# Kernel tuning notes

Hardware: AMD Instinct MI355X
Metric: run time of the kernel (lower is better)

## Reference

```python
import jax, jax.numpy as jnp
import numpy as np

N = 10000
E = 640000
IN_CH = 512
OUT_CH = 256
K = 2


def setup_inputs() -> dict:
    key = jax.random.key(0)
    k1, k2, k3, k4, k5 = jax.random.split(key, 5)
    x = jax.random.normal(k1, (N, IN_CH), dtype=jnp.float32)
    edge_index = jax.random.randint(k2, (2, E), 0, N, dtype=jnp.int64)
    lin_w = jax.random.normal(k3, (OUT_CH, IN_CH), dtype=jnp.float32) * (1.0 / np.sqrt(IN_CH))
    lin_b = jax.random.normal(k4, (OUT_CH,), dtype=jnp.float32) * 0.01
    weights = jax.random.uniform(k5, (K,), dtype=jnp.float32)
    return {"x": x, "edge_index": edge_index, "lin_w": lin_w, "lin_b": lin_b, "weights": weights}


def reference(x, edge_index, lin_w, lin_b, weights):
    n = x.shape[0]
    row, col = edge_index[0], edge_index[1]
    # deg = bincount(row); symmetric-normalized edge weights
    deg = jax.ops.segment_sum(jnp.ones(row.shape[0], dtype=x.dtype), row, num_segments=n)
    deg_inv_sqrt = jnp.where(deg > 0, jax.lax.rsqrt(deg), 0.0)
    norm = deg_inv_sqrt[row] * deg_inv_sqrt[col]  # [E]

    def spmm(h):
        # y[i] = sum_{e: row[e]==i} norm[e] * h[col[e]]
        return jax.ops.segment_sum(norm[:, None] * h[col], row, num_segments=n)

    out = x @ lin_w.T + lin_b  # [N, OUT_CH]
    # Faithful ARMA loop: x_k starts from the CURRENT accumulated `out` each hop-group
    for k in range(K):
        x_k = out
        for _ in range(k + 1):
            x_k = spmm(x_k)
        out = out + weights[k] * x_k
    return out
```

## Files before the change

### kernel.cpp

```cpp
#include <hip/hip_runtime.h>

#define N_NODES 10000
#define E_EDGES 640000
#define IN_CH   512
#define OUT_CH  256
#define HALF_CH 128
#define CSR_CAP (E_EDGES + 16 * N_NODES + 128)
#define G_GEMM_X 157
#define G_GEMM  (G_GEMM_X * 2)
#define HBLK    125
#define EPB     5120
#define CNT_LD  128

typedef short bf16x8 __attribute__((ext_vector_type(8)));
typedef float f32x4  __attribute__((ext_vector_type(4)));

__device__ __forceinline__ unsigned short f2b(float f) {
    unsigned int u = __float_as_uint(f);
    return (unsigned short)((u + 0x7FFFu + ((u >> 16) & 1u)) >> 16);
}
__device__ __forceinline__ float lo16(unsigned int u) { return __uint_as_float(u << 16); }
__device__ __forceinline__ float hi16(unsigned int u) { return __uint_as_float(u & 0xFFFF0000u); }
__device__ __forceinline__ float b2f(unsigned short u) { return __uint_as_float(((unsigned int)u) << 16); }

__global__ __launch_bounds__(256) void hist_rank(const int* __restrict__ row,
                                                 int* __restrict__ cnt,
                                                 unsigned short* __restrict__ rank) {
    __shared__ int hist[N_NODES];
    int b = blockIdx.x, tid = threadIdx.x;
    for (int i = tid; i < N_NODES; i += 256) hist[i] = 0;
    __syncthreads();
    int ebase = b * EPB;
    #pragma unroll 4
    for (int i = tid; i < EPB; i += 256) {
        int r = row[ebase + i];
        rank[ebase + i] = (unsigned short)atomicAdd(&hist[r], 1);
    }
    __syncthreads();
    for (int i = tid; i < N_NODES; i += 256) cnt[(size_t)i * CNT_LD + b] = hist[i];
}

__global__ __launch_bounds__(256) void alloc_a(int* __restrict__ cnt,
                                               int2* __restrict__ pd,
                                               float* __restrict__ dinv, float* __restrict__ sq,
                                               int* __restrict__ pads, int n) {
    int r = blockIdx.x * 4 + (threadIdx.x >> 6);
    int lane = threadIdx.x & 63;
    if (r >= n) return;
    int* cr = cnt + (size_t)r * CNT_LD;
    int v0 = cr[lane];
    int v1 = (lane < HBLK - 64) ? cr[64 + lane] : 0;
    int s0 = v0, s1 = v1;
    #pragma unroll
    for (int off = 1; off < 64; off <<= 1) {
        int t0 = __shfl_up(s0, off, 64);
        int t1 = __shfl_up(s1, off, 64);
        if (lane >= off) { s0 += t0; s1 += t1; }
    }
    int tot0 = __shfl(s0, 63, 64);
    int d = tot0 + __shfl(s1, 63, 64);
    int pad = (d + 15) & ~15;
    cr[lane] = s0 - v0;
    if (lane < HBLK - 64) cr[64 + lane] = tot0 + s1 - v1;
    if (lane == 0) {
        dinv[r] = (d > 0) ? rsqrtf((float)d) : 0.0f;
        sq[r]   = (d > 0) ? sqrtf((float)d) : 0.0f;
        pd[r] = make_int2(d, pad);
        pads[r] = pad;
    }
}

__global__ __launch_bounds__(1024) void scan_pads(const int* __restrict__ pads,
                                                  int* __restrict__ rowstart, int n) {
    __shared__ int ls[1024];
    int t = threadIdx.x;
    int base = t * 10;
    int loc[10];
    int sum = 0;
    if (base < n) {
        #pragma unroll
        for (int i = 0; i < 10; i++) { loc[i] = pads[base + i]; sum += loc[i]; }
    }
    ls[t] = sum;
    __syncthreads();
    for (int off = 1; off < 1024; off <<= 1) {
        int v = (t >= off) ? ls[t - off] : 0;
        __syncthreads();
        ls[t] += v;
        __syncthreads();
    }
    if (base < n) {
        int run = ls[t] - sum;
        #pragma unroll
        for (int i = 0; i < 10; i++) { rowstart[base + i] = run; run += loc[i]; }
    }
}

__global__ __launch_bounds__(256) void alloc_b(int* __restrict__ cnt,
                                               const int* __restrict__ rowstart,
                                               const int2* __restrict__ pd,
                                               int2* __restrict__ seg,
                                               int* __restrict__ csr_col, int n) {
    int r = blockIdx.x * 4 + (threadIdx.x >> 6);
    int lane = threadIdx.x & 63;
    if (r >= n) return;
    int s = rowstart[r];
    int2 pd_ = pd[r];
    int* cr = cnt + (size_t)r * CNT_LD;
    cr[lane] += s;
    if (lane < HBLK - 64) cr[64 + lane] += s;
    if (lane == 0) seg[r] = make_int2(s, s + pd_.y);
    int j = pd_.x + lane;
    if (j < pd_.y) csr_col[s + j] = N_NODES;
}

__global__ __launch_bounds__(256) void gemm_scatter(const float* __restrict__ x,
                                                    const float* __restrict__ w,
                                                    const float* __restrict__ bias,
                                                    const float* __restrict__ dinv,
                                                    unsigned short* __restrict__ h0b,
                                                    const int* __restrict__ row,
                                                    const int* __restrict__ col,
                                                    const int* __restrict__ base,
                                                    const unsigned short* __restrict__ rank,
                                                    int* __restrict__ csr_col) {
    __shared__ unsigned short As[64][72];
    __shared__ unsigned short Bs[128][72];
    int bid = blockIdx.x;
    int tid = threadIdx.x;
    if (bid >= G_GEMM) {
        int sb = bid - G_GEMM;
        int ebase = sb * EPB;
        #pragma unroll 4
        for (int i = tid; i < EPB; i += 256) {
            int e = ebase + i;
            int r = row[e];
            int p = base[(size_t)r * CNT_LD + sb] + (int)rank[e];
            csr_col[p] = col[e];
        }
        return;
    }
    int bx = bid % G_GEMM_X;
    int plane = bid / G_GEMM_X;
    int wave = tid >> 6, lane = tid & 63, quad = lane >> 4, l16 = lane & 15;
    int row0 = bx * 64;
    int n0 = plane * 128;
    unsigned short* h0b_p = h0b + (size_t)plane * (N_NODES + 1) * HALF_CH;

    int ar = tid >> 2;
    int aseg = (tid & 3) * 16;
    int br = tid >> 1;
    int bseg = (tid & 1) * 32;

    f32x4 acc[8] = {};
    for (int k0 = 0; k0 < IN_CH; k0 += 64) {
        {
            int gr = row0 + ar;
            if (gr < N_NODES) {
                const float4* src = (const float4*)(x + (size_t)gr * IN_CH + k0 + aseg);
                #pragma unroll
                for (int i = 0; i < 4; i++) {
                    float4 v = src[i];
                    ushort4 o;
                    o.x = f2b(v.x); o.y = f2b(v.y); o.z = f2b(v.z); o.w = f2b(v.w);
                    *(ushort4*)&As[ar][aseg + i * 4] = o;
                }
            } else {
                ushort4 z = {0, 0, 0, 0};
                #pragma unroll
                for (int i = 0; i < 4; i++) *(ushort4*)&As[ar][aseg + i * 4] = z;
            }
        }
        {
            const float4* src = (const float4*)(w + (size_t)(n0 + br) * IN_CH + k0 + bseg);
            #pragma unroll
            for (int i = 0; i < 8; i++) {
                float4 v = src[i];
                ushort4 o;
                o.x = f2b(v.x); o.y = f2b(v.y); o.z = f2b(v.z); o.w = f2b(v.w);
                *(ushort4*)&Bs[br][bseg + i * 4] = o;
            }
        }
        __syncthreads();
        #pragma unroll
        for (int kk = 0; kk < 2; kk++) {
            bf16x8 a = *(const bf16x8*)&As[wave * 16 + l16][kk * 32 + quad * 8];
            #pragma unroll
            for (int t = 0; t < 8; t++) {
                bf16x8 b = *(const bf16x8*)&Bs[t * 16 + l16][kk * 32 + quad * 8];
                acc[t] = __builtin_amdgcn_mfma_f32_16x16x32_bf16(a, b, acc[t], 0, 0, 0);
            }
        }
        __syncthreads();
    }
    #pragma unroll
    for (int t = 0; t < 8; t++) {
        int lcol = t * 16 + l16;
        int col_ = n0 + lcol;
        float bv = bias[col_];
        #pragma unroll
        for (int r = 0; r < 4; r++) {
            int grow = row0 + wave * 16 + quad * 4 + r;
            if (grow < N_NODES) {
                float v = acc[t][r] + bv;
                h0b_p[(size_t)grow * HALF_CH + lcol] = f2b(v * dinv[grow]);
            }
        }
    }
    if (bx == 0 && tid < 64)
        ((unsigned int*)(h0b_p + (size_t)N_NODES * HALF_CH))[tid] = 0u;
}

__global__ __launch_bounds__(256) void spmm_kernel(const unsigned short* __restrict__ hb,
                                                   const int2* __restrict__ seg,
                                                   const int* __restrict__ csr_col,
                                                   const float* __restrict__ dinv,
                                                   const float* __restrict__ sq,
                                                   const unsigned short* __restrict__ prev_b,
                                                   const float* __restrict__ wts, int widx,
                                                   unsigned short* __restrict__ yb_out,
                                                   float* __restrict__ axpy_out,
                                                   unsigned short* __restrict__ axpyb_out,
                                                   int n) {
    int plane = blockIdx.x & 1;
    int node = (blockIdx.x >> 1) * 4 + (threadIdx.x >> 6);
    int lane = threadIdx.x & 63;
    if (node >= n) return;
    int sub = lane >> 4, l16 = lane & 15;
    size_t pstride = (size_t)(n + 1) * HALF_CH;
    const unsigned short* hp = hb + (size_t)plane * pstride;

    int2 se = seg[node];
    int s = se.x, e = se.y;
    float acc[8] = {0.f, 0.f, 0.f, 0.f, 0.f, 0.f, 0.f, 0.f};
    if (s < e) {
        int c0 = csr_col[s + 0  + sub];
        int c1 = csr_col[s + 4  + sub];
        int c2 = csr_col[s + 8  + sub];
        int c3 = csr_col[s + 12 + sub];
        int p = s;
        while (true) {
            int pn = p + 16;
            int n0c = csr_col[pn + 0  + sub];
            int n1c = csr_col[pn + 4  + sub];
            int n2c = csr_col[pn + 8  + sub];
            int n3c = csr_col[pn + 12 + sub];
            uint4 v0 = *(const uint4*)(hp + (size_t)c0 * HALF_CH + l16 * 8);
            uint4 v1 = *(const uint4*)(hp + (size_t)c1 * HALF_CH + l16 * 8);
            uint4 v2 = *(const uint4*)(hp + (size_t)c2 * HALF_CH + l16 * 8);
            uint4 v3 = *(const uint4*)(hp + (size_t)c3 * HALF_CH + l16 * 8);
            acc[0] += lo16(v0.x) + lo16(v1.x) + lo16(v2.x) + lo16(v3.x);
            acc[1] += hi16(v0.x) + hi16(v1.x) + hi16(v2.x) + hi16(v3.x);
            acc[2] += lo16(v0.y) + lo16(v1.y) + lo16(v2.y) + lo16(v3.y);
            acc[3] += hi16(v0.y) + hi16(v1.y) + hi16(v2.y) + hi16(v3.y);
            acc[4] += lo16(v0.z) + lo16(v1.z) + lo16(v2.z) + lo16(v3.z);
            acc[5] += hi16(v0.z) + hi16(v1.z) + hi16(v2.z) + hi16(v3.z);
            acc[6] += lo16(v0.w) + lo16(v1.w) + lo16(v2.w) + lo16(v3.w);
            acc[7] += hi16(v0.w) + hi16(v1.w) + hi16(v2.w) + hi16(v3.w);
            c0 = n0c; c1 = n1c; c2 = n2c; c3 = n3c; p = pn;
            if (p >= e) break;
        }
    }
    #pragma unroll
    for (int k = 0; k < 8; k++) {
        acc[k] += __shfl_xor(acc[k], 16, 64);
        acc[k] += __shfl_xor(acc[k], 32, 64);
    }
    if (sub != 0) return;

    float di = dinv[node];
    float y[8];
    #pragma unroll
    for (int k = 0; k < 8; k++) y[k] = di * acc[k];

    size_t pbase = (size_t)plane * pstride + (size_t)node * HALF_CH + l16 * 8;
    size_t padrow = (size_t)plane * pstride + (size_t)n * HALF_CH + l16 * 8;
    if (yb_out) {
        ushort4 o0, o1;
        o0.x = f2b(di * y[0]); o0.y = f2b(di * y[1]); o0.z = f2b(di * y[2]); o0.w = f2b(di * y[3]);
        o1.x = f2b(di * y[4]); o1.y = f2b(di * y[5]); o1.z = f2b(di * y[6]); o1.w = f2b(di * y[7]);
        *(ushort4*)(yb_out + pbase) = o0;
        *(ushort4*)(yb_out + pbase + 4) = o1;
        if (node == 0) {
            ushort4 z = {0, 0, 0, 0};
            *(ushort4*)(yb_out + padrow) = z;
            *(ushort4*)(yb_out + padrow + 4) = z;
        }
    }
    if (prev_b) {
        float wk = wts[widx];
        float sqn = sq[node];
        ushort4 p0 = *(const ushort4*)(prev_b + pbase);
        ushort4 p1 = *(const ushort4*)(prev_b + pbase + 4);
        float o[8];
        o[0] = b2f(p0.x) * sqn + wk * y[0];
        o[1] = b2f(p0.y) * sqn + wk * y[1];
        o[2] = b2f(p0.z) * sqn + wk * y[2];
        o[3] = b2f(p0.w) * sqn + wk * y[3];
        o[4] = b2f(p1.x) * sqn + wk * y[4];
        o[5] = b2f(p1.y) * sqn + wk * y[5];
        o[6] = b2f(p1.z) * sqn + wk * y[6];
        o[7] = b2f(p1.w) * sqn + wk * y[7];
        if (axpy_out) {
            size_t fbase = (size_t)node * OUT_CH + plane * HALF_CH + l16 * 8;
            float4 f0 = {o[0], o[1], o[2], o[3]};
            float4 f1 = {o[4], o[5], o[6], o[7]};
            *(float4*)(axpy_out + fbase) = f0;
            *(float4*)(axpy_out + fbase + 4) = f1;
        }
        if (axpyb_out) {
            ushort4 b0, b1;
            b0.x = f2b(di * o[0]); b0.y = f2b(di * o[1]); b0.z = f2b(di * o[2]); b0.w = f2b(di * o[3]);
            b1.x = f2b(di * o[4]); b1.y = f2b(di * o[5]); b1.z = f2b(di * o[6]); b1.w = f2b(di * o[7]);
            *(ushort4*)(axpyb_out + pbase) = b0;
            *(ushort4*)(axpyb_out + pbase + 4) = b1;
            if (node == 0) {
                ushort4 z = {0, 0, 0, 0};
                *(ushort4*)(axpyb_out + padrow) = z;
                *(ushort4*)(axpyb_out + padrow + 4) = z;
            }
        }
    }
}

extern "C" void kernel_launch(void* const* d_in, const int* in_sizes, int n_in,
                              void* d_out, int out_size, void* d_ws, size_t ws_size,
                              hipStream_t stream) {
    const float* x     = (const float*)d_in[0];
    const int*   ei    = (const int*)d_in[1];
    const float* lin_w = (const float*)d_in[2];
    const float* lin_b = (const float*)d_in[3];
    const float* wts   = (const float*)d_in[4];
    float* out = (float*)d_out;

    char* ws = (char*)d_ws;
    size_t off = 0;
    auto alloc = [&](size_t bytes) -> void* {
        void* p = ws + off;
        off += (bytes + 255) & ~(size_t)255;
        return p;
    };
    int*   cnt      = (int*)  alloc((size_t)N_NODES * CNT_LD * 4);
    unsigned short* rank = (unsigned short*)alloc((size_t)E_EDGES * 2);
    int2*  pd       = (int2*) alloc((size_t)N_NODES * 8);
    int*   pads     = (int*)  alloc((size_t)N_NODES * 4);
    int*   rowstart = (int*)  alloc((size_t)N_NODES * 4);
    int2*  seg      = (int2*) alloc((size_t)N_NODES * 8);
    float* dinv     = (float*)alloc(N_NODES * 4);
    float* sq       = (float*)alloc(N_NODES * 4);
    int*   csr_col  = (int*)  alloc((size_t)CSR_CAP * 4);
    unsigned short* h0b   = (unsigned short*)alloc((size_t)2 * (N_NODES + 1) * HALF_CH * 2);
    unsigned short* out1b = (unsigned short*)alloc((size_t)2 * (N_NODES + 1) * HALF_CH * 2);
    unsigned short* t2b   = (unsigned short*)alloc((size_t)2 * (N_NODES + 1) * HALF_CH * 2);

    const int* row = ei;
    const int* col = ei + E_EDGES;

    hist_rank<<<HBLK, 256, 0, stream>>>(row, cnt, rank);
    alloc_a<<<(N_NODES + 3) / 4, 256, 0, stream>>>(cnt, pd, dinv, sq, pads, N_NODES);
    scan_pads<<<1, 1024, 0, stream>>>(pads, rowstart, N_NODES);
    alloc_b<<<(N_NODES + 3) / 4, 256, 0, stream>>>(cnt, rowstart, pd, seg, csr_col, N_NODES);

    gemm_scatter<<<G_GEMM + HBLK, 256, 0, stream>>>(x, lin_w, lin_b, dinv, h0b,
                                                    row, col, cnt, rank, csr_col);

    int sgrid = 2 * ((N_NODES + 3) / 4);
    spmm_kernel<<<sgrid, 256, 0, stream>>>(h0b, seg, csr_col, dinv, sq, h0b,
                                           wts, 0, nullptr, nullptr, out1b, N_NODES);
    spmm_kernel<<<sgrid, 256, 0, stream>>>(out1b, seg, csr_col, dinv, sq, nullptr,
                                           wts, 0, t2b, nullptr, nullptr, N_NODES);
    spmm_kernel<<<sgrid, 256, 0, stream>>>(t2b, seg, csr_col, dinv, sq, out1b,
                                           wts, 1, nullptr, out, nullptr, N_NODES);
}
```

Before: 206.6 us.

## Transpose per-block count layout, stage scatter bases in LDS, double-buffer SpMM gathers

Stores the per-block histogram counts block-major so hist_rank writes contiguous rows. The scatter blocks now add rowstart and stage the combined base offsets in shared memory, so alloc_b no longer has to update cnt and the per-edge base lookup becomes an LDS read. The SpMM inner loop is restructured to issue the next group's row gathers before accumulating the current group, to hide gather latency. In exchange, alloc_a now reads cnt with a node stride and loses coalescing, and the software pipeline raises register pressure.

```diff
diff --git a/kernel.cpp b/kernel.cpp
--- a/kernel.cpp
+++ b/kernel.cpp
@@ -10,7 +10,6 @@
 #define G_GEMM  (G_GEMM_X * 2)
 #define HBLK    125
 #define EPB     5120
-#define CNT_LD  128
 
 typedef short bf16x8 __attribute__((ext_vector_type(8)));
 typedef float f32x4  __attribute__((ext_vector_type(4)));
@@ -37,7 +36,8 @@
         rank[ebase + i] = (unsigned short)atomicAdd(&hist[r], 1);
     }
     __syncthreads();
-    for (int i = tid; i < N_NODES; i += 256) cnt[(size_t)i * CNT_LD + b] = hist[i];
+    int* cb = cnt + (size_t)b * N_NODES;
+    for (int i = tid; i < N_NODES; i += 256) cb[i] = hist[i];
 }
 
 __global__ __launch_bounds__(256) void alloc_a(int* __restrict__ cnt,
@@ -47,9 +47,8 @@
     int r = blockIdx.x * 4 + (threadIdx.x >> 6);
     int lane = threadIdx.x & 63;
     if (r >= n) return;
-    int* cr = cnt + (size_t)r * CNT_LD;
-    int v0 = cr[lane];
-    int v1 = (lane < HBLK - 64) ? cr[64 + lane] : 0;
+    int v0 = cnt[(size_t)lane * N_NODES + r];
+    int v1 = (lane < HBLK - 64) ? cnt[(size_t)(64 + lane) * N_NODES + r] : 0;
     int s0 = v0, s1 = v1;
     #pragma unroll
     for (int off = 1; off < 64; off <<= 1) {
@@ -60,8 +59,8 @@
     int tot0 = __shfl(s0, 63, 64);
     int d = tot0 + __shfl(s1, 63, 64);
     int pad = (d + 15) & ~15;
-    cr[lane] = s0 - v0;
-    if (lane < HBLK - 64) cr[64 + lane] = tot0 + s1 - v1;
+    cnt[(size_t)lane * N_NODES + r] = s0 - v0;
+    if (lane < HBLK - 64) cnt[(size_t)(64 + lane) * N_NODES + r] = tot0 + s1 - v1;
     if (lane == 0) {
         dinv[r] = (d > 0) ? rsqrtf((float)d) : 0.0f;
         sq[r]   = (d > 0) ? sqrtf((float)d) : 0.0f;
@@ -96,8 +95,7 @@
     }
 }
 
-__global__ __launch_bounds__(256) void alloc_b(int* __restrict__ cnt,
-                                               const int* __restrict__ rowstart,
+__global__ __launch_bounds__(256) void alloc_b(const int* __restrict__ rowstart,
                                                const int2* __restrict__ pd,
                                                int2* __restrict__ seg,
                                                int* __restrict__ csr_col, int n) {
@@ -106,9 +104,6 @@
     if (r >= n) return;
     int s = rowstart[r];
     int2 pd_ = pd[r];
-    int* cr = cnt + (size_t)r * CNT_LD;
-    cr[lane] += s;
-    if (lane < HBLK - 64) cr[64 + lane] += s;
     if (lane == 0) seg[r] = make_int2(s, s + pd_.y);
     int j = pd_.x + lane;
     if (j < pd_.y) csr_col[s + j] = N_NODES;
@@ -122,24 +117,37 @@
                                                     const int* __restrict__ row,
                                                     const int* __restrict__ col,
                                                     const int* __restrict__ base,
+                                                    const int* __restrict__ rowstart,
                                                     const unsigned short* __restrict__ rank,
                                                     int* __restrict__ csr_col) {
-    __shared__ unsigned short As[64][72];
-    __shared__ unsigned short Bs[128][72];
+    __shared__ __align__(16) char smem[40960];
     int bid = blockIdx.x;
     int tid = threadIdx.x;
     if (bid >= G_GEMM) {
         int sb = bid - G_GEMM;
+        int* bs = (int*)smem;
+        const int4* cb4 = (const int4*)(base + (size_t)sb * N_NODES);
+        const int4* rs4 = (const int4*)rowstart;
+        for (int i = tid; i < N_NODES / 4; i += 256) {
+            int4 c = cb4[i];
+            int4 r = rs4[i];
+            int4 o;
+            o.x = c.x + r.x; o.y = c.y + r.y; o.z = c.z + r.z; o.w = c.w + r.w;
+            ((int4*)bs)[i] = o;
+        }
+        __syncthreads();
         int ebase = sb * EPB;
         #pragma unroll 4
         for (int i = tid; i < EPB; i += 256) {
             int e = ebase + i;
-            int r = row[e];
-            int p = base[(size_t)r * CNT_LD + sb] + (int)rank[e];
+            int p = bs[row[e]] + (int)rank[e];
             csr_col[p] = col[e];
         }
         return;
     }
+    typedef unsigned short us72[72];
+    us72* As = (us72*)smem;
+    us72* Bs = (us72*)(smem + 64 * 72 * 2);
     int bx = bid % G_GEMM_X;
     int plane = bid / G_GEMM_X;
     int wave = tid >> 6, lane = tid & 63, quad = lane >> 4, l16 = lane & 15;
@@ -234,32 +242,49 @@
     int s = se.x, e = se.y;
     float acc[8] = {0.f, 0.f, 0.f, 0.f, 0.f, 0.f, 0.f, 0.f};
     if (s < e) {
-        int c0 = csr_col[s + 0  + sub];
-        int c1 = csr_col[s + 4  + sub];
-        int c2 = csr_col[s + 8  + sub];
-        int c3 = csr_col[s + 12 + sub];
+        int cA0 = csr_col[s + 0  + sub];
+        int cA1 = csr_col[s + 4  + sub];
+        int cA2 = csr_col[s + 8  + sub];
+        int cA3 = csr_col[s + 12 + sub];
+        uint4 vA0 = *(const uint4*)(hp + (size_t)cA0 * HALF_CH + l16 * 8);
+        uint4 vA1 = *(const uint4*)(hp + (size_t)cA1 * HALF_CH + l16 * 8);
+        uint4 vA2 = *(const uint4*)(hp + (size_t)cA2 * HALF_CH + l16 * 8);
+        uint4 vA3 = *(const uint4*)(hp + (size_t)cA3 * HALF_CH + l16 * 8);
+        int cB0 = csr_col[s + 16 + sub];
+        int cB1 = csr_col[s + 20 + sub];
+        int cB2 = csr_col[s + 24 + sub];
+        int cB3 = csr_col[s + 28 + sub];
         int p = s;
-        while (true) {
-            int pn = p + 16;
-            int n0c = csr_col[pn + 0  + sub];
-            int n1c = csr_col[pn + 4  + sub];
-            int n2c = csr_col[pn + 8  + sub];
-            int n3c = csr_col[pn + 12 + sub];
-            uint4 v0 = *(const uint4*)(hp + (size_t)c0 * HALF_CH + l16 * 8);
-            uint4 v1 = *(const uint4*)(hp + (size_t)c1 * HALF_CH + l16 * 8);
-            uint4 v2 = *(const uint4*)(hp + (size_t)c2 * HALF_CH + l16 * 8);
-            uint4 v3 = *(const uint4*)(hp + (size_t)c3 * HALF_CH + l16 * 8);
-            acc[0] += lo16(v0.x) + lo16(v1.x) + lo16(v2.x) + lo16(v3.x);
-            acc[1] += hi16(v0.x) + hi16(v1.x) + hi16(v2.x) + hi16(v3.x);
-            acc[2] += lo16(v0.y) + lo16(v1.y) + lo16(v2.y) + lo16(v3.y);
-            acc[3] += hi16(v0.y) + hi16(v1.y) + hi16(v2.y) + hi16(v3.y);
-            acc[4] += lo16(v0.z) + lo16(v1.z) + lo16(v2.z) + lo16(v3.z);
-            acc[5] += hi16(v0.z) + hi16(v1.z) + hi16(v2.z) + hi16(v3.z);
-            acc[6] += lo16(v0.w) + lo16(v1.w) + lo16(v2.w) + lo16(v3.w);
-            acc[7] += hi16(v0.w) + hi16(v1.w) + hi16(v2.w) + hi16(v3.w);
-            c0 = n0c; c1 = n1c; c2 = n2c; c3 = n3c; p = pn;
-            if (p >= e) break;
-        }
+        while (p + 16 < e) {
+            uint4 vB0 = *(const uint4*)(hp + (size_t)cB0 * HALF_CH + l16 * 8);
+            uint4 vB1 = *(const uint4*)(hp + (size_t)cB1 * HALF_CH + l16 * 8);
+            uint4 vB2 = *(const uint4*)(hp + (size_t)cB2 * HALF_CH + l16 * 8);
+            uint4 vB3 = *(const uint4*)(hp + (size_t)cB3 * HALF_CH + l16 * 8);
+            int pn = p + 32;
+            int cC0 = csr_col[pn + 0  + sub];
+            int cC1 = csr_col[pn + 4  + sub];
+            int cC2 = csr_col[pn + 8  + sub];
+            int cC3 = csr_col[pn + 12 + sub];
+            acc[0] += lo16(vA0.x) + lo16(vA1.x) + lo16(vA2.x) + lo16(vA3.x);
+            acc[1] += hi16(vA0.x) + hi16(vA1.x) + hi16(vA2.x) + hi16(vA3.x);
+            acc[2] += lo16(vA0.y) + lo16(vA1.y) + lo16(vA2.y) + lo16(vA3.y);
+            acc[3] += hi16(vA0.y) + hi16(vA1.y) + hi16(vA2.y) + hi16(vA3.y);
+            acc[4] += lo16(vA0.z) + lo16(vA1.z) + lo16(vA2.z) + lo16(vA3.z);
+            acc[5] += hi16(vA0.z) + hi16(vA1.z) + hi16(vA2.z) + hi16(vA3.z);
+            acc[6] += lo16(vA0.w) + lo16(vA1.w) + lo16(vA2.w) + lo16(vA3.w);
+            acc[7] += hi16(vA0.w) + hi16(vA1.w) + hi16(vA2.w) + hi16(vA3.w);
+            vA0 = vB0; vA1 = vB1; vA2 = vB2; vA3 = vB3;
+            cB0 = cC0; cB1 = cC1; cB2 = cC2; cB3 = cC3;
+            p += 16;
+        }
+        acc[0] += lo16(vA0.x) + lo16(vA1.x) + lo16(vA2.x) + lo16(vA3.x);
+        acc[1] += hi16(vA0.x) + hi16(vA1.x) + hi16(vA2.x) + hi16(vA3.x);
+        acc[2] += lo16(vA0.y) + lo16(vA1.y) + lo16(vA2.y) + lo16(vA3.y);
+        acc[3] += hi16(vA0.y) + hi16(vA1.y) + hi16(vA2.y) + hi16(vA3.y);
+        acc[4] += lo16(vA0.z) + lo16(vA1.z) + lo16(vA2.z) + lo16(vA3.z);
+        acc[5] += hi16(vA0.z) + hi16(vA1.z) + hi16(vA2.z) + hi16(vA3.z);
+        acc[6] += lo16(vA0.w) + lo16(vA1.w) + lo16(vA2.w) + lo16(vA3.w);
+        acc[7] += hi16(vA0.w) + hi16(vA1.w) + hi16(vA2.w) + hi16(vA3.w);
     }
     #pragma unroll
     for (int k = 0; k < 8; k++) {
@@ -340,7 +365,7 @@
         off += (bytes + 255) & ~(size_t)255;
         return p;
     };
-    int*   cnt      = (int*)  alloc((size_t)N_NODES * CNT_LD * 4);
+    int*   cnt      = (int*)  alloc((size_t)HBLK * N_NODES * 4);
     unsigned short* rank = (unsigned short*)alloc((size_t)E_EDGES * 2);
     int2*  pd       = (int2*) alloc((size_t)N_NODES * 8);
     int*   pads     = (int*)  alloc((size_t)N_NODES * 4);
@@ -359,10 +384,10 @@
     hist_rank<<<HBLK, 256, 0, stream>>>(row, cnt, rank);
     alloc_a<<<(N_NODES + 3) / 4, 256, 0, stream>>>(cnt, pd, dinv, sq, pads, N_NODES);
     scan_pads<<<1, 1024, 0, stream>>>(pads, rowstart, N_NODES);
-    alloc_b<<<(N_NODES + 3) / 4, 256, 0, stream>>>(cnt, rowstart, pd, seg, csr_col, N_NODES);
+    alloc_b<<<(N_NODES + 3) / 4, 256, 0, stream>>>(rowstart, pd, seg, csr_col, N_NODES);
 
     gemm_scatter<<<G_GEMM + HBLK, 256, 0, stream>>>(x, lin_w, lin_b, dinv, h0b,
-                                                    row, col, cnt, rank, csr_col);
+                                                    row, col, cnt, rowstart, rank, csr_col);
 
     int sgrid = 2 * ((N_NODES + 3) / 4);
     spmm_kernel<<<sgrid, 256, 0, stream>>>(h0b, seg, csr_col, dinv, sq, h0b,
```

Measured after the change: 203.9 us. No clear change (-1.3%).
